# Kernel optimization log

Measured on AMD Instinct MI355X. Metric: run time of the kernel, lower is better.

Reference implementation:

```python
import jax, jax.numpy as jnp
import numpy as np

N = 20000      # nodes
E = 320000     # edges (avg degree 16)
G = 256        # graphs
F_NODE = 64
F_EDGE = 16
HID = 256
H, C = 4, 64   # heads, per-head channels
EPS = 1e-5


def setup_inputs() -> dict:
    key = jax.random.key(0)
    ks = jax.random.split(key, 24)
    def rn(k, shape, scale=0.05):
        return jax.random.normal(k, shape, dtype=jnp.float32) * scale
    src = jax.random.randint(ks[0], (E,), 0, N)
    dst = (src + 1 + jax.random.randint(ks[1], (E,), 0, N - 1)) % N  # no pre-existing self loops
    edge_index = jnp.stack([src, dst]).astype(jnp.int32)
    batch = ((jnp.arange(N) * G) // N).astype(jnp.int32)  # contiguous graph ids, all G graphs non-empty
    return {
        'x': rn(ks[2], (N, F_NODE), 1.0),
        'edge_index': edge_index,
        'batch': batch,
        'edge_attr': rn(ks[3], (E, F_EDGE), 1.0),
        'enc_W': rn(ks[4], (F_NODE, HID)),
        'enc_b': jnp.zeros((HID,), jnp.float32),
        'conv_Wl': rn(ks[5], (3, HID, HID)),
        'conv_bl': rn(ks[6], (3, HID)),
        'conv_Wr': rn(ks[7], (3, HID, HID)),
        'conv_br': rn(ks[8], (3, HID)),
        'conv_We': rn(ks[9], (3, F_EDGE, HID)),
        'conv_att': rn(ks[10], (3, H, C)),
        'conv_bias': rn(ks[11], (3, HID)),
        'bn_gamma': jnp.ones((3, HID), jnp.float32),
        'bn_beta': jnp.zeros((3, HID), jnp.float32),
        'bn_mean': rn(ks[12], (3, HID)),
        'bn_var': jax.random.uniform(ks[13], (3, HID), dtype=jnp.float32) + 0.5,
        'cls_W1': rn(ks[14], (2 * HID, HID)),
        'cls_b1': jnp.zeros((HID,), jnp.float32),
        'cls_g1': jnp.ones((HID,), jnp.float32),
        'cls_bt1': jnp.zeros((HID,), jnp.float32),
        'cls_m1': rn(ks[15], (HID,)),
        'cls_v1': jax.random.uniform(ks[16], (HID,), dtype=jnp.float32) + 0.5,
        'cls_W2': rn(ks[17], (HID, HID // 2)),
        'cls_b2': jnp.zeros((HID // 2,), jnp.float32),
        'cls_g2': jnp.ones((HID // 2,), jnp.float32),
        'cls_bt2': jnp.zeros((HID // 2,), jnp.float32),
        'cls_m2': rn(ks[18], (HID // 2,)),
        'cls_v2': jax.random.uniform(ks[19], (HID // 2,), dtype=jnp.float32) + 0.5,
        'cls_W3': rn(ks[20], (HID // 2, 1)),
        'cls_b3': jnp.zeros((1,), jnp.float32),
    }


def _bn(v, g, b, m, var):
    return (v - m) * jax.lax.rsqrt(var + EPS) * g + b


def _gatv2(h, src, dst, eattr, Wl, bl, Wr, br, We, att, bias, n):
    # GATv2Conv (share_weights=False, concat=True) with edge features.
    xl = (h @ Wl + bl).reshape(n, H, C)          # messages come from lin_l(source)
    xr = (h @ Wr + br).reshape(n, H, C)
    ef = (eattr @ We).reshape(-1, H, C)
    z = jax.nn.leaky_relu(xl[src] + xr[dst] + ef, 0.2)   # [E', H, C]
    alpha = jnp.einsum('ehc,hc->eh', z, att)             # [E', H]
    amax = jax.ops.segment_max(alpha, dst, num_segments=n)
    amax = jnp.where(jnp.isfinite(amax), amax, 0.0)
    ex = jnp.exp(alpha - amax[dst])
    den = jax.ops.segment_sum(ex, dst, num_segments=n)
    a = ex / den[dst]                                    # self loops guarantee den > 0
    out = jax.ops.segment_sum(a[:, :, None] * xl[src], dst, num_segments=n)
    return out.reshape(n, H * C) + bias


def reference(x, edge_index, batch, edge_attr, enc_W, enc_b, conv_Wl, conv_bl, conv_Wr, conv_br, conv_We, conv_att, conv_bias, bn_gamma, bn_beta, bn_mean, bn_var, cls_W1, cls_b1, cls_g1, cls_bt1, cls_m1, cls_v1, cls_W2, cls_b2, cls_g2, cls_bt2, cls_m2, cls_v2, cls_W3, cls_b3):
    n = x.shape[0]
    src, dst = edge_index[0], edge_index[1]
    # add self loops with fill_value='mean' (mean of incoming edge_attr per node)
    deg = jax.ops.segment_sum(jnp.ones(src.shape, x.dtype), dst, num_segments=n)
    loop_attr = jax.ops.segment_sum(edge_attr, dst, num_segments=n) / jnp.maximum(deg, 1.0)[:, None]
    loop = jnp.arange(n, dtype=src.dtype)
    src2 = jnp.concatenate([src, loop])
    dst2 = jnp.concatenate([dst, loop])
    ea2 = jnp.concatenate([edge_attr, loop_attr], axis=0)

    h = jax.nn.relu(x @ enc_W + enc_b)
    for i in range(3):  # fixed layer count
        h_in = h
        hc = _gatv2(h, src2, dst2, ea2, conv_Wl[i], conv_bl[i], conv_Wr[i], conv_br[i], conv_We[i], conv_att[i], conv_bias[i], n)
        h = jax.nn.relu(_bn(hc, bn_gamma[i], bn_beta[i], bn_mean[i], bn_var[i])) + h_in

    cnt = jax.ops.segment_sum(jnp.ones((n,), h.dtype), batch, num_segments=G)
    x_mean = jax.ops.segment_sum(h, batch, num_segments=G) / jnp.maximum(cnt, 1.0)[:, None]
    x_max = jax.ops.segment_max(h, batch, num_segments=G)
    xp = jnp.concatenate([x_mean, x_max], axis=1)

    z = jax.nn.relu(_bn(xp @ cls_W1 + cls_b1, cls_g1, cls_bt1, cls_m1, cls_v1))
    z = jax.nn.relu(_bn(z @ cls_W2 + cls_b2, cls_g2, cls_bt2, cls_m2, cls_v2))
    return (z @ cls_W3 + cls_b3)[:, 0]
```

## Files before the change

kernel.cpp:

```cpp
#include <hip/hip_runtime.h>
#include <hip/hip_bf16.h>

#define N_NODES 20000
#define N_EDGES 320000
#define N_E2    (N_EDGES + N_NODES)
#define N_GRAPHS 256
#define HID 256
#define EPS 1e-5f
#define NSCAN 20
#define CPB 2

typedef unsigned short u16;
typedef __attribute__((ext_vector_type(8))) short short8;
typedef __attribute__((ext_vector_type(4))) float f32x4;

__device__ __forceinline__ float b2f(u16 u) {
    union { unsigned int i; float f; } v; v.i = ((unsigned int)u) << 16; return v.f;
}
__device__ __forceinline__ u16 f2b(float f) {
    __hip_bfloat16 h = __float2bfloat16(f);
    return *reinterpret_cast<u16*>(&h);
}

__global__ void k_count(const int* __restrict__ dst, int* __restrict__ cnt) {
    int e = blockIdx.x * 256 + threadIdx.x;
    if (e < N_EDGES) atomicAdd(&cnt[dst[e]], 1);
}

__global__ void k_scan1(const int* __restrict__ cnt, int* __restrict__ rowp, int* __restrict__ part) {
    __shared__ int ls[256];
    int b = blockIdx.x, tid = threadIdx.x;
    int base = b * 1024 + tid * 4;
    int c[4]; int s = 0;
#pragma unroll
    for (int u = 0; u < 4; u++) { int i = base + u; c[u] = (i < N_NODES) ? cnt[i] + 1 : 0; s += c[u]; }
    ls[tid] = s; __syncthreads();
    for (int off = 1; off < 256; off <<= 1) {
        int v = (tid >= off) ? ls[tid - off] : 0;
        __syncthreads();
        ls[tid] += v;
        __syncthreads();
    }
    int excl = ls[tid] - s;
#pragma unroll
    for (int u = 0; u < 4; u++) { int i = base + u; if (i < N_NODES) rowp[i] = excl; excl += c[u]; }
    if (tid == 255) part[b] = ls[255];
}

__global__ void k_scan2(int* part, int* rowp) {
    int s = 0;
    for (int b = 0; b < NSCAN; b++) { int v = part[b]; part[b] = s; s += v; }
    rowp[N_NODES] = s;
}

__global__ void k_scan3(int* __restrict__ rowp, const int* __restrict__ part) {
    int b = blockIdx.x, tid = threadIdx.x;
    int add = part[b];
    int base = b * 1024 + tid * 4;
#pragma unroll
    for (int u = 0; u < 4; u++) { int i = base + u; if (i < N_NODES) rowp[i] += add; }
}

__global__ void k_fill(const int* __restrict__ src, const int* __restrict__ dst,
                       const int* __restrict__ rowp, int* __restrict__ cursor,
                       int* __restrict__ csr_src, int* __restrict__ csr_dst,
                       int* __restrict__ csr_aid) {
    int t = blockIdx.x * 256 + threadIdx.x;
    if (t < N_EDGES) {
        int d = dst[t];
        int pos = atomicAdd(&cursor[d], 1);
        int w = rowp[d] + pos;
        csr_src[w] = src[t];
        csr_dst[w] = d;
        csr_aid[w] = t;
    } else if (t < N_E2) {
        int n = t - N_EDGES;
        int pos = atomicAdd(&cursor[n], 1);
        int w = rowp[n] + pos;
        csr_src[w] = n;
        csr_dst[w] = n;
        csr_aid[w] = N_EDGES + n;
    } else if (t < N_E2 + 512) {
        csr_src[t] = 0;
        csr_dst[t] = 0;
    }
}

__global__ void k_eacsr(const int* __restrict__ csr_aid, const int* __restrict__ rowp,
                        const float* __restrict__ edge_attr,
                        u16* __restrict__ ea_bf) {
    int t = blockIdx.x * 256 + threadIdx.x;
    if (t >= N_E2 * 2) return;
    int e = t >> 1, hf = t & 1;
    int aid = csr_aid[e];
    float v[8];
    if (aid < N_EDGES) {
        const float4* ap = (const float4*)(edge_attr + (size_t)aid * 16 + hf * 8);
        float4 a = ap[0], b = ap[1];
        v[0] = a.x; v[1] = a.y; v[2] = a.z; v[3] = a.w;
        v[4] = b.x; v[5] = b.y; v[6] = b.z; v[7] = b.w;
    } else {
        int n = aid - N_EDGES;
        int st = rowp[n], en = rowp[n + 1];
        float s[8] = {0.f, 0.f, 0.f, 0.f, 0.f, 0.f, 0.f, 0.f};
        for (int i = st; i < en; i++) {
            int a2 = csr_aid[i];
            if (a2 < N_EDGES) {
                const float4* ap = (const float4*)(edge_attr + (size_t)a2 * 16 + hf * 8);
                float4 a = ap[0], b = ap[1];
                s[0] += a.x; s[1] += a.y; s[2] += a.z; s[3] += a.w;
                s[4] += b.x; s[5] += b.y; s[6] += b.z; s[7] += b.w;
            }
        }
        float rdeg = 1.0f / fmaxf((float)(en - st - 1), 1.0f);
#pragma unroll
        for (int q = 0; q < 8; q++) v[q] = s[q] * rdeg;
    }
    u16 o[8];
#pragma unroll
    for (int q = 0; q < 8; q++) o[q] = f2b(v[q]);
    *(uint4*)(ea_bf + (size_t)t * 8) = *(uint4*)o;
}

__global__ void k_wef(const float* __restrict__ We, u16* __restrict__ Wef) {
    int t = blockIdx.x * 256 + threadIdx.x;
    if (t >= 3 * 16 * 64) return;
    int layer = t >> 10, r = t & 1023;
    int nt = r >> 6, l = r & 63;
    int kc = l >> 4, ch = nt * 16 + (l & 15);
    u16 v[8];
#pragma unroll
    for (int q = 0; q < 8; q++) {
        float x = 0.f;
        if (kc < 2) x = We[(size_t)layer * 4096 + (size_t)(kc * 8 + q) * 256 + ch];
        v[q] = f2b(x);
    }
    *(uint4*)(Wef + (size_t)t * 8) = *(uint4*)v;
}

__global__ void k_xbf(const float* __restrict__ x, u16* __restrict__ xb) {
    int t = blockIdx.x * 256 + threadIdx.x;
    if (t >= N_NODES * 16) return;
    float4 v = ((const float4*)x)[t];
    u16 o[4] = {f2b(v.x), f2b(v.y), f2b(v.z), f2b(v.w)};
    *(ushort4*)(xb + (size_t)t * 4) = *(ushort4*)o;
}

__global__ void k_twg(const float* __restrict__ W, u16* __restrict__ Wt, int K, int N,
                      unsigned int lstride) {
    __shared__ float tile[32][33];
    int layer = blockIdx.z;
    const float* Wp = W + (size_t)layer * K * N;
    u16* Wtp = Wt + (size_t)layer * lstride;
    int bk = blockIdx.x * 32, bn = blockIdx.y * 32;
    int tx = threadIdx.x & 31, ty = threadIdx.x >> 5;
#pragma unroll
    for (int q = 0; q < 4; q++) {
        int k = bk + ty + q * 8;
        tile[ty + q * 8][tx] = Wp[(size_t)k * N + bn + tx];
    }
    __syncthreads();
#pragma unroll
    for (int q = 0; q < 4; q++) {
        int n = bn + ty + q * 8;
        Wtp[(size_t)n * K + bk + tx] = f2b(tile[tx][ty + q * 8]);
    }
}

__global__ void k_blr(const float* __restrict__ bl, const float* __restrict__ br,
                      float* __restrict__ blr) {
    int t = blockIdx.x * 256 + threadIdx.x;
    if (t >= 3 * 512) return;
    int l = t >> 9, c = t & 511;
    blr[t] = (c < 256) ? bl[l * 256 + c] : br[l * 256 + (c - 256)];
}

template <int EPI>
__global__ __launch_bounds__(256) void k_gemm_bf(
    const u16* __restrict__ A, int lda,
    const u16* __restrict__ Bt, int ldb, int K,
    const float* __restrict__ bias,
    u16* __restrict__ Cbf, int ldc, int coff,
    float* __restrict__ Cf, int M)
{
    __shared__ __align__(16) u16 As[128 * 40];
    __shared__ __align__(16) u16 Bs[64 * 40];
    int tid = threadIdx.x;
    int lane = tid & 63, w = tid >> 6;
    int m0 = blockIdx.x * 128, n0 = blockIdx.y * 64;

    f32x4 acc[2][4];
#pragma unroll
    for (int i = 0; i < 2; i++)
#pragma unroll
        for (int j = 0; j < 4; j++) acc[i][j] = (f32x4){0.f, 0.f, 0.f, 0.f};

    int srow = tid >> 2, skc = (tid & 3) * 8;
    int lr = lane & 15, lk = (lane >> 4) * 8;

    int ktiles = K >> 5;
    for (int kt = 0; kt < ktiles; kt++) {
        if (kt) __syncthreads();
#pragma unroll
        for (int q = 0; q < 2; q++) {
            int arow = q * 64 + srow;
            uint4 av = make_uint4(0, 0, 0, 0);
            if (m0 + arow < M)
                av = *(const uint4*)(A + (size_t)(m0 + arow) * lda + kt * 32 + skc);
            *(uint4*)&As[arow * 40 + skc] = av;
        }
        {
            uint4 bv = *(const uint4*)(Bt + (size_t)(n0 + srow) * ldb + kt * 32 + skc);
            *(uint4*)&Bs[srow * 40 + skc] = bv;
        }
        __syncthreads();

        short8 af0 = *(const short8*)&As[(w * 32 + lr) * 40 + lk];
        short8 af1 = *(const short8*)&As[(w * 32 + 16 + lr) * 40 + lk];
        short8 bf[4];
#pragma unroll
        for (int nt = 0; nt < 4; nt++)
            bf[nt] = *(const short8*)&Bs[(nt * 16 + lr) * 40 + lk];
#pragma unroll
        for (int nt = 0; nt < 4; nt++) {
            acc[0][nt] = __builtin_amdgcn_mfma_f32_16x16x32_bf16(af0, bf[nt], acc[0][nt], 0, 0, 0);
            acc[1][nt] = __builtin_amdgcn_mfma_f32_16x16x32_bf16(af1, bf[nt], acc[1][nt], 0, 0, 0);
        }
    }

    int rq = (lane >> 4) * 4;
#pragma unroll
    for (int nt = 0; nt < 4; nt++) {
        int col = n0 + nt * 16 + lr;
        float bv = bias[col];
#pragma unroll
        for (int mt = 0; mt < 2; mt++) {
#pragma unroll
            for (int j = 0; j < 4; j++) {
                int row = m0 + w * 32 + mt * 16 + rq + j;
                if (row < M) {
                    float v = acc[mt][nt][j] + bv;
                    if (EPI == 1) {
                        v = fmaxf(v, 0.f);
                        Cf[(size_t)row * ldc + col] = v;
                        Cbf[(size_t)row * ldc + col] = f2b(v);
                    } else {
                        Cbf[(size_t)row * ldc + coff + col] = f2b(v);
                    }
                }
            }
        }
    }
}

__global__ __launch_bounds__(256) void k_alpha3(
    const u16* __restrict__ xlr,
    const u16* __restrict__ ea_bf,
    const int* __restrict__ csr_src, const int* __restrict__ csr_dst,
    const u16* __restrict__ Wef,
    const float* __restrict__ att,
    float* __restrict__ alpha)
{
    __shared__ __align__(16) u16 wef_s[16 * 64 * 8];
    int tid = threadIdx.x, lane = tid & 63, w = tid >> 6;
    {
        const uint4* s = (const uint4*)Wef;
        uint4* d = (uint4*)wef_s;
#pragma unroll
        for (int q = 0; q < 4; q++) d[q * 256 + tid] = s[q * 256 + tid];
    }
    int eg = lane >> 4, t16 = lane & 15;

    float att_r[16];
#pragma unroll
    for (int q = 0; q < 16; q++) att_r[q] = att[q * 16 + t16];
    __syncthreads();

    for (int it = 0; it < CPB; it++) {
        int chunk = blockIdx.x * CPB + it;
        if (chunk * 64 >= N_E2) break;
        int e_base = chunk * 64 + w * 16;

        short8 afrag = {0, 0, 0, 0, 0, 0, 0, 0};
        if (eg < 2) {
            int e = e_base + t16; if (e > N_E2 - 1) e = N_E2 - 1;
            afrag = *(const short8*)(ea_bf + (size_t)e * 16 + eg * 8);
        }
        int4 s4 = *(const int4*)(csr_src + e_base + eg * 4);
        int4 d4 = *(const int4*)(csr_dst + e_base + eg * 4);
        const u16* xlp[4]; const u16* xrp[4];
        xlp[0] = xlr + (size_t)s4.x * 512;       xlp[1] = xlr + (size_t)s4.y * 512;
        xlp[2] = xlr + (size_t)s4.z * 512;       xlp[3] = xlr + (size_t)s4.w * 512;
        xrp[0] = xlr + (size_t)d4.x * 512 + 256; xrp[1] = xlr + (size_t)d4.y * 512 + 256;
        xrp[2] = xlr + (size_t)d4.z * 512 + 256; xrp[3] = xlr + (size_t)d4.w * 512 + 256;

        float pj[4] = {0.f, 0.f, 0.f, 0.f};
#pragma unroll
        for (int nt = 0; nt < 16; nt++) {
            short8 bfrag = *(const short8*)&wef_s[(nt * 64 + lane) * 8];
            f32x4 D = __builtin_amdgcn_mfma_f32_16x16x32_bf16(
                afrag, bfrag, (f32x4){0.f, 0.f, 0.f, 0.f}, 0, 0, 0);
            int ch = nt * 16 + t16;
#pragma unroll
            for (int j = 0; j < 4; j++) {
                float z = D[j] + b2f(xlp[j][ch]) + b2f(xrp[j][ch]);
                z = fmaxf(z, 0.f) + 0.2f * fminf(z, 0.f);
                pj[j] = fmaf(z, att_r[nt], pj[j]);
            }
            if ((nt & 3) == 3) {
                int hh = nt >> 2;
#pragma unroll
                for (int j = 0; j < 4; j++) {
                    float p = pj[j];
                    p += __shfl_xor(p, 1, 64);
                    p += __shfl_xor(p, 2, 64);
                    p += __shfl_xor(p, 4, 64);
                    p += __shfl_xor(p, 8, 64);
                    int e = e_base + eg * 4 + j;
                    if (t16 == 0 && e < N_E2) alpha[(size_t)e * 4 + hh] = p;
                    pj[j] = 0.f;
                }
            }
        }
    }
}

__global__ __launch_bounds__(256) void k_aggr(
    const u16* __restrict__ xlr, const float* __restrict__ alpha,
    const int* __restrict__ rowp, const int* __restrict__ csr_src,
    const float* __restrict__ cbias,
    const float* __restrict__ bng, const float* __restrict__ bnb,
    const float* __restrict__ bnm, const float* __restrict__ bnv,
    float* __restrict__ h, u16* __restrict__ h_bf)
{
    __shared__ float lex[4][64][4];
    __shared__ int   lsrc[4][64];
    int lane = threadIdx.x & 63;
    int wv = threadIdx.x >> 6;
    int n = blockIdx.x * 4 + wv;
    if (n >= N_NODES) return;
    int st = rowp[n], en = rowp[n + 1];
    int hsel = lane >> 4;
    int c0 = lane * 4;

    float m4[4]  = {-3.0e38f, -3.0e38f, -3.0e38f, -3.0e38f};
    float den4[4] = {0.f, 0.f, 0.f, 0.f};
    float acc[4]  = {0.f, 0.f, 0.f, 0.f};

    for (int cs = st; cs < en; cs += 64) {
        int cnt = min(64, en - cs);
        float a4[4];
        int s_i = 0;
        if (lane < cnt) {
            float4 v = *(const float4*)(alpha + (size_t)(cs + lane) * 4);
            a4[0] = v.x; a4[1] = v.y; a4[2] = v.z; a4[3] = v.w;
            s_i = csr_src[cs + lane];
        } else {
            a4[0] = a4[1] = a4[2] = a4[3] = -3.0e38f;
        }
        float cm[4] = {a4[0], a4[1], a4[2], a4[3]};
#pragma unroll
        for (int o = 32; o >= 1; o >>= 1)
#pragma unroll
            for (int u = 0; u < 4; u++) cm[u] = fmaxf(cm[u], __shfl_xor(cm[u], o, 64));
        float sc[4];
#pragma unroll
        for (int u = 0; u < 4; u++) {
            float nm = fmaxf(m4[u], cm[u]);
            sc[u] = __expf(m4[u] - nm);
            den4[u] *= sc[u];
            m4[u] = nm;
        }
        float scl = sc[hsel];
#pragma unroll
        for (int u = 0; u < 4; u++) acc[u] *= scl;
        float ex[4];
#pragma unroll
        for (int u = 0; u < 4; u++) ex[u] = (lane < cnt) ? __expf(a4[u] - m4[u]) : 0.f;
        float sx[4] = {ex[0], ex[1], ex[2], ex[3]};
#pragma unroll
        for (int o = 32; o >= 1; o >>= 1)
#pragma unroll
            for (int u = 0; u < 4; u++) sx[u] += __shfl_xor(sx[u], o, 64);
#pragma unroll
        for (int u = 0; u < 4; u++) den4[u] += sx[u];
        *(float4*)&lex[wv][lane][0] = make_float4(ex[0], ex[1], ex[2], ex[3]);
        lsrc[wv][lane] = s_i;
        int j = 0;
        for (; j + 8 <= cnt; j += 8) {
            float a[8]; int sj[8];
#pragma unroll
            for (int q = 0; q < 8; q++) { a[q] = lex[wv][j + q][hsel]; sj[q] = lsrc[wv][j + q]; }
            ushort4 xg[8];
#pragma unroll
            for (int q = 0; q < 8; q++) xg[q] = *(const ushort4*)(xlr + (size_t)sj[q] * 512 + c0);
#pragma unroll
            for (int q = 0; q < 8; q++) {
                acc[0] += a[q] * b2f(((const u16*)&xg[q])[0]);
                acc[1] += a[q] * b2f(((const u16*)&xg[q])[1]);
                acc[2] += a[q] * b2f(((const u16*)&xg[q])[2]);
                acc[3] += a[q] * b2f(((const u16*)&xg[q])[3]);
            }
        }
        for (; j < cnt; j++) {
            float a = lex[wv][j][hsel];
            int sj = lsrc[wv][j];
            ushort4 xg = *(const ushort4*)(xlr + (size_t)sj * 512 + c0);
            acc[0] += a * b2f(((const u16*)&xg)[0]);
            acc[1] += a * b2f(((const u16*)&xg)[1]);
            acc[2] += a * b2f(((const u16*)&xg)[2]);
            acc[3] += a * b2f(((const u16*)&xg)[3]);
        }
    }

    float dd = den4[hsel];
    float4 hin = *(const float4*)(h + (size_t)n * 256 + c0);
    float4 cb  = *(const float4*)(cbias + c0);
    float4 gg  = *(const float4*)(bng + c0);
    float4 bb  = *(const float4*)(bnb + c0);
    float4 mm  = *(const float4*)(bnm + c0);
    float4 vv  = *(const float4*)(bnv + c0);
    float hi[4] = {hin.x, hin.y, hin.z, hin.w};
    float cbv[4] = {cb.x, cb.y, cb.z, cb.w};
    float gv[4] = {gg.x, gg.y, gg.z, gg.w};
    float bv[4] = {bb.x, bb.y, bb.z, bb.w};
    float mv[4] = {mm.x, mm.y, mm.z, mm.w};
    float vvv[4] = {vv.x, vv.y, vv.z, vv.w};
    float4 o;
    ushort4 ob;
#pragma unroll
    for (int u = 0; u < 4; u++) {
        float val = acc[u] / dd + cbv[u];
        val = (val - mv[u]) * rsqrtf(vvv[u] + EPS) * gv[u] + bv[u];
        val = fmaxf(val, 0.f) + hi[u];
        ((float*)&o)[u] = val;
        ((u16*)&ob)[u] = f2b(val);
    }
    *(float4*)(h + (size_t)n * 256 + c0) = o;
    *(ushort4*)(h_bf + (size_t)n * 256 + c0) = ob;
}

__global__ __launch_bounds__(256) void k_poolp(
    const float* __restrict__ h, float* __restrict__ psum, float* __restrict__ pmax)
{
    int g = blockIdx.x, p = blockIdx.y, c = threadIdx.x;
    int gst = (g * N_NODES + N_GRAPHS - 1) / N_GRAPHS;
    int gen = ((g + 1) * N_NODES + N_GRAPHS - 1) / N_GRAPHS;
    int len = gen - gst;
    int cst = gst + (len * p) / 8;
    int cen = gst + (len * (p + 1)) / 8;
    float s = 0.f, mx = -3.0e38f;
    for (int i = cst; i < cen; i++) {
        float v = h[(size_t)i * 256 + c];
        s += v;
        mx = fmaxf(mx, v);
    }
    psum[(size_t)(g * 8 + p) * 256 + c] = s;
    pmax[(size_t)(g * 8 + p) * 256 + c] = mx;
}

__global__ __launch_bounds__(256) void k_head(
    const float* __restrict__ psum, const float* __restrict__ pmax,
    const float* __restrict__ W1, const float* __restrict__ b1,
    const float* __restrict__ g1, const float* __restrict__ bt1,
    const float* __restrict__ m1, const float* __restrict__ v1,
    const float* __restrict__ W2, const float* __restrict__ b2,
    const float* __restrict__ g2, const float* __restrict__ bt2,
    const float* __restrict__ m2, const float* __restrict__ v2,
    const float* __restrict__ W3, const float* __restrict__ b3,
    float* __restrict__ out)
{
    __shared__ float xp_s[512];
    __shared__ float z1_s[256];
    __shared__ float z2p[2][128];
    __shared__ float z2_s[128];
    int g = blockIdx.x, c = threadIdx.x;
    int gst = (g * N_NODES + N_GRAPHS - 1) / N_GRAPHS;
    int gen = ((g + 1) * N_NODES + N_GRAPHS - 1) / N_GRAPHS;

    float s = 0.f, mx = -3.0e38f;
#pragma unroll
    for (int p = 0; p < 8; p++) {
        s += psum[(size_t)(g * 8 + p) * 256 + c];
        mx = fmaxf(mx, pmax[(size_t)(g * 8 + p) * 256 + c]);
    }
    xp_s[c] = s / (float)(gen - gst);
    xp_s[256 + c] = mx;
    __syncthreads();

    float a0 = 0.f, a1 = 0.f, a2 = 0.f, a3 = 0.f;
#pragma unroll 4
    for (int k = 0; k < 512; k += 4) {
        a0 = fmaf(xp_s[k + 0], W1[(k + 0) * 256 + c], a0);
        a1 = fmaf(xp_s[k + 1], W1[(k + 1) * 256 + c], a1);
        a2 = fmaf(xp_s[k + 2], W1[(k + 2) * 256 + c], a2);
        a3 = fmaf(xp_s[k + 3], W1[(k + 3) * 256 + c], a3);
    }
    float a = (a0 + a1) + (a2 + a3) + b1[c];
    a = (a - m1[c]) * rsqrtf(v1[c] + EPS) * g1[c] + bt1[c];
    z1_s[c] = fmaxf(a, 0.f);
    __syncthreads();

    {
        int c2 = c & 127, half = c >> 7;
        float b_acc = 0.f;
#pragma unroll 4
        for (int k = 0; k < 128; k++) {
            int kk = half * 128 + k;
            b_acc = fmaf(z1_s[kk], W2[kk * 128 + c2], b_acc);
        }
        z2p[half][c2] = b_acc;
    }
    __syncthreads();
    if (c < 128) {
        float a2v = z2p[0][c] + z2p[1][c] + b2[c];
        a2v = (a2v - m2[c]) * rsqrtf(v2[c] + EPS) * g2[c] + bt2[c];
        z2_s[c] = fmaxf(a2v, 0.f);
    }
    __syncthreads();

    if (c < 64) {
        float a3v = z2_s[c] * W3[c] + z2_s[c + 64] * W3[c + 64];
#pragma unroll
        for (int o = 32; o >= 1; o >>= 1) a3v += __shfl_xor(a3v, o, 64);
        if (c == 0) out[g] = a3v + b3[0];
    }
}

extern "C" void kernel_launch(void* const* d_in, const int* in_sizes, int n_in,
                              void* d_out, int out_size, void* d_ws, size_t ws_size,
                              hipStream_t stream) {
    const float* x         = (const float*)d_in[0];
    const int*   ei        = (const int*)d_in[1];
    const int*   src       = ei;
    const int*   dst       = ei + N_EDGES;
    const float* edge_attr = (const float*)d_in[3];
    const float* enc_W     = (const float*)d_in[4];
    const float* enc_b     = (const float*)d_in[5];
    const float* conv_Wl   = (const float*)d_in[6];
    const float* conv_bl   = (const float*)d_in[7];
    const float* conv_Wr   = (const float*)d_in[8];
    const float* conv_br   = (const float*)d_in[9];
    const float* conv_We   = (const float*)d_in[10];
    const float* conv_att  = (const float*)d_in[11];
    const float* conv_bias = (const float*)d_in[12];
    const float* bn_g      = (const float*)d_in[13];
    const float* bn_b      = (const float*)d_in[14];
    const float* bn_m      = (const float*)d_in[15];
    const float* bn_v      = (const float*)d_in[16];
    const float* cls_W1    = (const float*)d_in[17];
    const float* cls_b1    = (const float*)d_in[18];
    const float* cls_g1    = (const float*)d_in[19];
    const float* cls_bt1   = (const float*)d_in[20];
    const float* cls_m1    = (const float*)d_in[21];
    const float* cls_v1    = (const float*)d_in[22];
    const float* cls_W2    = (const float*)d_in[23];
    const float* cls_b2    = (const float*)d_in[24];
    const float* cls_g2    = (const float*)d_in[25];
    const float* cls_bt2   = (const float*)d_in[26];
    const float* cls_m2    = (const float*)d_in[27];
    const float* cls_v2    = (const float*)d_in[28];
    const float* cls_W3    = (const float*)d_in[29];
    const float* cls_b3    = (const float*)d_in[30];
    float* out = (float*)d_out;

    char* ws = (char*)d_ws;
    size_t off = 0;
    auto alloc = [&](size_t bytes) -> void* {
        void* p = ws + off;
        off += (bytes + 255) & ~(size_t)255;
        return p;
    };
    float* h       = (float*)alloc((size_t)N_NODES * 256 * 4);
    u16*   h_bf    = (u16*)alloc((size_t)N_NODES * 256 * 2);
    u16*   xlr_bf  = (u16*)alloc((size_t)N_NODES * 512 * 2);
    u16*   ea_bf   = (u16*)alloc((size_t)N_E2 * 16 * 2);
    float* alphas  = (float*)alloc((size_t)N_E2 * 4 * 4);
    u16*   x_bf    = (u16*)alloc((size_t)N_NODES * 64 * 2);
    u16*   enc_Wt  = (u16*)alloc((size_t)64 * 256 * 2);
    u16*   Wtlr    = (u16*)alloc((size_t)3 * 512 * 256 * 2);
    float* blr     = (float*)alloc((size_t)3 * 512 * 4);
    u16*   Wef     = (u16*)alloc((size_t)3 * 16 * 64 * 8 * 2);
    float* psum    = (float*)alloc((size_t)N_GRAPHS * 8 * 256 * 4);
    float* pmax    = (float*)alloc((size_t)N_GRAPHS * 8 * 256 * 4);
    int*   cntcur  = (int*)alloc((size_t)2 * N_NODES * 4);
    int*   cnt     = cntcur;
    int*   cursor  = cntcur + N_NODES;
    int*   rowp    = (int*)alloc((size_t)(N_NODES + 1) * 4);
    int*   csr_src = (int*)alloc((size_t)(N_E2 + 512) * 4);
    int*   csr_dst = (int*)alloc((size_t)(N_E2 + 512) * 4);
    int*   csr_aid = (int*)alloc((size_t)N_E2 * 4);
    int*   part    = (int*)alloc(64 * 4);

    hipMemsetAsync(cntcur, 0, (size_t)2 * N_NODES * 4, stream);
    k_count<<<(N_EDGES + 255) / 256, 256, 0, stream>>>(dst, cnt);
    k_scan1<<<NSCAN, 256, 0, stream>>>(cnt, rowp, part);
    k_scan2<<<1, 1, 0, stream>>>(part, rowp);
    k_scan3<<<NSCAN, 256, 0, stream>>>(rowp, part);
    k_fill<<<(N_E2 + 512 + 255) / 256, 256, 0, stream>>>(src, dst, rowp, cursor,
                                                         csr_src, csr_dst, csr_aid);
    k_eacsr<<<(N_E2 * 2 + 255) / 256, 256, 0, stream>>>(csr_aid, rowp, edge_attr, ea_bf);

    k_xbf<<<(N_NODES * 16 + 255) / 256, 256, 0, stream>>>(x, x_bf);
    k_twg<<<dim3(2, 8, 1), 256, 0, stream>>>(enc_W, enc_Wt, 64, 256, 64 * 256);
    k_twg<<<dim3(8, 8, 3), 256, 0, stream>>>(conv_Wl, Wtlr, 256, 256, 512 * 256);
    k_twg<<<dim3(8, 8, 3), 256, 0, stream>>>(conv_Wr, Wtlr + 256 * 256, 256, 256, 512 * 256);
    k_blr<<<6, 256, 0, stream>>>(conv_bl, conv_br, blr);
    k_wef<<<12, 256, 0, stream>>>(conv_We, Wef);

    dim3 ggrid((N_NODES + 127) / 128, 4);
    dim3 ggrid2((N_NODES + 127) / 128, 8);
    k_gemm_bf<1><<<ggrid, 256, 0, stream>>>(x_bf, 64, enc_Wt, 64, 64,
                                            enc_b, h_bf, 256, 0, h, N_NODES);

    int nchunks = (N_E2 + 63) / 64;
    int ablocks = (nchunks + CPB - 1) / CPB;
    for (int i = 0; i < 3; i++) {
        k_gemm_bf<0><<<ggrid2, 256, 0, stream>>>(h_bf, 256, Wtlr + (size_t)i * 131072, 256, 256,
                                                 blr + (size_t)i * 512, xlr_bf, 512, 0, nullptr, N_NODES);
        k_alpha3<<<ablocks, 256, 0, stream>>>(
            xlr_bf, ea_bf, csr_src, csr_dst,
            Wef + (size_t)i * 8192, conv_att + (size_t)i * 256, alphas);
        k_aggr<<<N_NODES / 4, 256, 0, stream>>>(
            xlr_bf, alphas, rowp, csr_src,
            conv_bias + (size_t)i * HID,
            bn_g + (size_t)i * HID, bn_b + (size_t)i * HID,
            bn_m + (size_t)i * HID, bn_v + (size_t)i * HID, h, h_bf);
    }

    k_poolp<<<dim3(N_GRAPHS, 8), 256, 0, stream>>>(h, psum, pmax);
    k_head<<<N_GRAPHS, 256, 0, stream>>>(
        psum, pmax, cls_W1, cls_b1, cls_g1, cls_bt1, cls_m1, cls_v1,
        cls_W2, cls_b2, cls_g2, cls_bt2, cls_m2, cls_v2,
        cls_W3, cls_b3, out);
}
```

Before: 432.7 us.

## Drop softmax max-subtraction; compute exp and denominators via atomics in alpha kernel

The alpha kernel now exponentiates attention logits directly and accumulates per-destination softmax denominators with global atomicAdd. The aggregation kernel no longer does the online max/rescale and the warp-wide shuffle reductions; it reads precomputed exp weights and the denominator. This removes reduction and exp work from the aggregation pass. In exchange it adds a memset and contended atomics, and it gives up the max-subtraction that guards against exp overflow, which relies on the logits staying small.

```diff
diff --git a/kernel.cpp b/kernel.cpp
--- a/kernel.cpp
+++ b/kernel.cpp
@@ -259,7 +259,8 @@
     const int* __restrict__ csr_src, const int* __restrict__ csr_dst,
     const u16* __restrict__ Wef,
     const float* __restrict__ att,
-    float* __restrict__ alpha)
+    float* __restrict__ exw,
+    float* __restrict__ den)
 {
     __shared__ __align__(16) u16 wef_s[16 * 64 * 8];
     int tid = threadIdx.x, lane = tid & 63, w = tid >> 6;
@@ -288,6 +289,7 @@
         }
         int4 s4 = *(const int4*)(csr_src + e_base + eg * 4);
         int4 d4 = *(const int4*)(csr_dst + e_base + eg * 4);
+        int darr[4] = {d4.x, d4.y, d4.z, d4.w};
         const u16* xlp[4]; const u16* xrp[4];
         xlp[0] = xlr + (size_t)s4.x * 512;       xlp[1] = xlr + (size_t)s4.y * 512;
         xlp[2] = xlr + (size_t)s4.z * 512;       xlp[3] = xlr + (size_t)s4.w * 512;
@@ -317,7 +319,11 @@
                     p += __shfl_xor(p, 4, 64);
                     p += __shfl_xor(p, 8, 64);
                     int e = e_base + eg * 4 + j;
-                    if (t16 == 0 && e < N_E2) alpha[(size_t)e * 4 + hh] = p;
+                    if (t16 == 0 && e < N_E2) {
+                        float ex = __expf(p);
+                        exw[(size_t)e * 4 + hh] = ex;
+                        atomicAdd(&den[(size_t)darr[j] * 4 + hh], ex);
+                    }
                     pj[j] = 0.f;
                 }
             }
@@ -326,7 +332,8 @@
 }
 
 __global__ __launch_bounds__(256) void k_aggr(
-    const u16* __restrict__ xlr, const float* __restrict__ alpha,
+    const u16* __restrict__ xlr, const float* __restrict__ exw,
+    const float* __restrict__ den,
     const int* __restrict__ rowp, const int* __restrict__ csr_src,
     const float* __restrict__ cbias,
     const float* __restrict__ bng, const float* __restrict__ bnb,
@@ -343,48 +350,17 @@
     int hsel = lane >> 4;
     int c0 = lane * 4;
 
-    float m4[4]  = {-3.0e38f, -3.0e38f, -3.0e38f, -3.0e38f};
-    float den4[4] = {0.f, 0.f, 0.f, 0.f};
-    float acc[4]  = {0.f, 0.f, 0.f, 0.f};
+    float acc[4] = {0.f, 0.f, 0.f, 0.f};
 
     for (int cs = st; cs < en; cs += 64) {
         int cnt = min(64, en - cs);
-        float a4[4];
+        float4 v = make_float4(0.f, 0.f, 0.f, 0.f);
         int s_i = 0;
         if (lane < cnt) {
-            float4 v = *(const float4*)(alpha + (size_t)(cs + lane) * 4);
-            a4[0] = v.x; a4[1] = v.y; a4[2] = v.z; a4[3] = v.w;
+            v = *(const float4*)(exw + (size_t)(cs + lane) * 4);
             s_i = csr_src[cs + lane];
-        } else {
-            a4[0] = a4[1] = a4[2] = a4[3] = -3.0e38f;
-        }
-        float cm[4] = {a4[0], a4[1], a4[2], a4[3]};
-#pragma unroll
-        for (int o = 32; o >= 1; o >>= 1)
-#pragma unroll
-            for (int u = 0; u < 4; u++) cm[u] = fmaxf(cm[u], __shfl_xor(cm[u], o, 64));
-        float sc[4];
-#pragma unroll
-        for (int u = 0; u < 4; u++) {
-            float nm = fmaxf(m4[u], cm[u]);
-            sc[u] = __expf(m4[u] - nm);
-            den4[u] *= sc[u];
-            m4[u] = nm;
-        }
-        float scl = sc[hsel];
-#pragma unroll
-        for (int u = 0; u < 4; u++) acc[u] *= scl;
-        float ex[4];
-#pragma unroll
-        for (int u = 0; u < 4; u++) ex[u] = (lane < cnt) ? __expf(a4[u] - m4[u]) : 0.f;
-        float sx[4] = {ex[0], ex[1], ex[2], ex[3]};
-#pragma unroll
-        for (int o = 32; o >= 1; o >>= 1)
-#pragma unroll
-            for (int u = 0; u < 4; u++) sx[u] += __shfl_xor(sx[u], o, 64);
-#pragma unroll
-        for (int u = 0; u < 4; u++) den4[u] += sx[u];
-        *(float4*)&lex[wv][lane][0] = make_float4(ex[0], ex[1], ex[2], ex[3]);
+        }
+        *(float4*)&lex[wv][lane][0] = v;
         lsrc[wv][lane] = s_i;
         int j = 0;
         for (; j + 8 <= cnt; j += 8) {
@@ -413,7 +389,7 @@
         }
     }
 
-    float dd = den4[hsel];
+    float dd = den[(size_t)n * 4 + hsel];
     float4 hin = *(const float4*)(h + (size_t)n * 256 + c0);
     float4 cb  = *(const float4*)(cbias + c0);
     float4 gg  = *(const float4*)(bng + c0);
@@ -575,7 +551,7 @@
     u16*   h_bf    = (u16*)alloc((size_t)N_NODES * 256 * 2);
     u16*   xlr_bf  = (u16*)alloc((size_t)N_NODES * 512 * 2);
     u16*   ea_bf   = (u16*)alloc((size_t)N_E2 * 16 * 2);
-    float* alphas  = (float*)alloc((size_t)N_E2 * 4 * 4);
+    float* exw     = (float*)alloc((size_t)N_E2 * 4 * 4);
     u16*   x_bf    = (u16*)alloc((size_t)N_NODES * 64 * 2);
     u16*   enc_Wt  = (u16*)alloc((size_t)64 * 256 * 2);
     u16*   Wtlr    = (u16*)alloc((size_t)3 * 512 * 256 * 2);
@@ -586,6 +562,7 @@
     int*   cntcur  = (int*)alloc((size_t)2 * N_NODES * 4);
     int*   cnt     = cntcur;
     int*   cursor  = cntcur + N_NODES;
+    float* den3    = (float*)alloc((size_t)3 * N_NODES * 4 * 4);
     int*   rowp    = (int*)alloc((size_t)(N_NODES + 1) * 4);
     int*   csr_src = (int*)alloc((size_t)(N_E2 + 512) * 4);
     int*   csr_dst = (int*)alloc((size_t)(N_E2 + 512) * 4);
@@ -593,6 +570,8 @@
     int*   part    = (int*)alloc(64 * 4);
 
     hipMemsetAsync(cntcur, 0, (size_t)2 * N_NODES * 4, stream);
+    hipMemsetAsync(den3, 0, (size_t)3 * N_NODES * 4 * 4, stream);
+
     k_count<<<(N_EDGES + 255) / 256, 256, 0, stream>>>(dst, cnt);
     k_scan1<<<NSCAN, 256, 0, stream>>>(cnt, rowp, part);
     k_scan2<<<1, 1, 0, stream>>>(part, rowp);
@@ -616,13 +595,14 @@
     int nchunks = (N_E2 + 63) / 64;
     int ablocks = (nchunks + CPB - 1) / CPB;
     for (int i = 0; i < 3; i++) {
+        float* den = den3 + (size_t)i * N_NODES * 4;
         k_gemm_bf<0><<<ggrid2, 256, 0, stream>>>(h_bf, 256, Wtlr + (size_t)i * 131072, 256, 256,
                                                  blr + (size_t)i * 512, xlr_bf, 512, 0, nullptr, N_NODES);
         k_alpha3<<<ablocks, 256, 0, stream>>>(
             xlr_bf, ea_bf, csr_src, csr_dst,
-            Wef + (size_t)i * 8192, conv_att + (size_t)i * 256, alphas);
+            Wef + (size_t)i * 8192, conv_att + (size_t)i * 256, exw, den);
         k_aggr<<<N_NODES / 4, 256, 0, stream>>>(
-            xlr_bf, alphas, rowp, csr_src,
+            xlr_bf, exw, den, rowp, csr_src,
             conv_bias + (size_t)i * HID,
             bn_g + (size_t)i * HID, bn_b + (size_t)i * HID,
             bn_m + (size_t)i * HID, bn_v + (size_t)i * HID, h, h_bf);
```

Result: slower. 525.4 us (+21.4%).
